# Kernel tuning notes

Hardware: AMD Instinct MI355X
Metric: run time of the kernel (lower is better)

Reference implementation:

```python
import jax, jax.numpy as jnp
import numpy as np

DIM = 768
H = 12
HD = 64  # head_dim = dim // num_heads
SCALE = HD ** (-0.5)
EPS = 1e-6


def setup_inputs() -> dict:
    key = jax.random.key(0)
    k1, k2, k3, k4, k5 = jax.random.split(key, 5)
    B, N = 8, 1024
    x = jax.random.normal(k1, (B, N, DIM), dtype=jnp.float32)
    policy = jax.random.uniform(k2, (B, N, 1), dtype=jnp.float32)
    # nn.Linear weights: [out_features, in_features]; qkv_bias=False, proj has bias
    qkv_w = jax.random.normal(k3, (3 * H * HD, DIM), dtype=jnp.float32) * (DIM ** -0.5)
    proj_w = jax.random.normal(k4, (DIM, H * HD), dtype=jnp.float32) * ((H * HD) ** -0.5)
    proj_b = jax.random.normal(k5, (DIM,), dtype=jnp.float32) * 0.01
    return {"x": x, "policy": policy, "qkv_w": qkv_w, "proj_w": proj_w, "proj_b": proj_b}


def _softmax_with_policy(attn, policy):
    # attn: [B,H,N,N], policy: [B,N,1]
    B, Hh, N, _ = attn.shape
    attn_policy = policy.reshape(B, 1, 1, N)
    eye = jnp.eye(N, dtype=attn_policy.dtype).reshape(1, 1, N, N)
    attn_policy = attn_policy + (1.0 - attn_policy) * eye
    max_att = jnp.max(attn, axis=-1, keepdims=True)
    a = jnp.exp((attn - max_att).astype(jnp.float32)) * attn_policy.astype(jnp.float32)
    a = (a + EPS / N) / (jnp.sum(a, axis=-1, keepdims=True) + EPS)
    return a.astype(max_att.dtype)


def reference(x, policy, qkv_w, proj_w, proj_b):
    B, N, C = x.shape
    qkv = (x @ qkv_w.T).reshape(B, N, 3, H, HD)
    qkv = jnp.transpose(qkv, (2, 0, 3, 1, 4))  # [3,B,H,N,HD]
    q, k, v = qkv[0], qkv[1], qkv[2]
    attn = jnp.einsum('bhnd,bhmd->bhnm', q * SCALE, k)  # [B,H,N,N]
    attn = _softmax_with_policy(attn, policy)
    out = jnp.einsum('bhnm,bhmd->bhnd', attn, v)  # [B,H,N,HD]
    out = jnp.transpose(out, (0, 2, 1, 3)).reshape(B, N, H * HD)
    return out @ proj_w.T + proj_b
```

## Files before the change

kernel.cpp:

```cpp
#include <hip/hip_runtime.h>

typedef __bf16 bf16x8 __attribute__((ext_vector_type(8)));
typedef float floatx4 __attribute__((ext_vector_type(4)));

#define EPSF 1e-6f

__device__ inline unsigned short f2bf(float f) {
  union { float f; unsigned u; } x; x.f = f;
  unsigned r = x.u + 0x7FFFu + ((x.u >> 16) & 1u);
  return (unsigned short)(r >> 16);
}
__device__ inline float bf2f(unsigned short u) {
  union { unsigned u; float f; } x; x.u = ((unsigned)u) << 16;
  return x.f;
}
__device__ inline unsigned pk2bf(float lo, float hi) {
  union { float f; unsigned u; } a, b; a.f = lo; b.f = hi;
  unsigned ua = a.u + 0x8000u, ub = b.u + 0x8000u;
  return (ub & 0xFFFF0000u) | (ua >> 16);
}
__device__ inline float fexp2(float x) { return __builtin_amdgcn_exp2f(x); }

__device__ inline floatx4 mfma16(bf16x8 a, bf16x8 b, floatx4 c) {
  return __builtin_amdgcn_mfma_f32_16x16x32_bf16(a, b, c, 0, 0, 0);
}

__device__ inline void gll16(const unsigned short* g, unsigned short* l) {
  __builtin_amdgcn_global_load_lds((__attribute__((address_space(1))) void*)g,
                                   (__attribute__((address_space(3))) void*)l, 16, 0, 0);
}

__device__ __host__ inline int sigma_inv(int p) {
  const int qq = p >> 3, jj = p & 7;
  return (jj < 4) ? (qq * 4 + jj) : (16 + qq * 4 + jj - 4);
}

__global__ __launch_bounds__(256) void prep_kernel(const float* __restrict__ x,
                                                   const float* __restrict__ qkv_w,
                                                   const float* __restrict__ proj_w,
                                                   const float* __restrict__ policy,
                                                   unsigned short* __restrict__ xb,
                                                   unsigned short* __restrict__ wqkv,
                                                   unsigned short* __restrict__ wproj,
                                                   unsigned short* __restrict__ pbf) {
  const int bid = blockIdx.x, tid = threadIdx.x;
  if (bid < 3072) {
    const int i = bid * 2048 + tid * 8;
    float4 v0 = *(const float4*)(x + i);
    float4 v1 = *(const float4*)(x + i + 4);
    __align__(16) unsigned short o[8] = {f2bf(v0.x), f2bf(v0.y), f2bf(v0.z), f2bf(v0.w),
                                         f2bf(v1.x), f2bf(v1.y), f2bf(v1.z), f2bf(v1.w)};
    *(float4*)(xb + i) = *(float4*)o;
  } else if (bid < 3936) {
    const int i = (bid - 3072) * 2048 + tid * 8;
    const float s = (i < 589824) ? 0.18033688011112042f : 1.0f;
    float4 v0 = *(const float4*)(qkv_w + i);
    float4 v1 = *(const float4*)(qkv_w + i + 4);
    __align__(16) unsigned short o[8] = {
        f2bf(v0.x * s), f2bf(v0.y * s), f2bf(v0.z * s), f2bf(v0.w * s),
        f2bf(v1.x * s), f2bf(v1.y * s), f2bf(v1.z * s), f2bf(v1.w * s)};
    *(float4*)(wqkv + i) = *(float4*)o;
  } else if (bid < 4224) {
    const int i0 = (bid - 3936) * 2048 + tid * 8;
    const int base = (i0 / 768) * 768 + ((i0 % 768) & ~63);
    __align__(16) unsigned short o[8];
#pragma unroll
    for (int t = 0; t < 8; t++) {
      const int cp = (i0 + t) & 63;
      const int c = 16 * (cp & 3) + (cp >> 2);
      o[t] = f2bf(proj_w[base + c]);
    }
    *(float4*)(wproj + i0) = *(float4*)o;
  } else {
    const int idx = (bid - 4224) * 256 + tid;
    const int b = idx >> 10, g = idx & 1023;
    const int c = ((g >> 5) << 5) + sigma_inv(g & 31);
    pbf[idx] = f2bf(policy[b * 1024 + c]);
  }
}

template <int EP, int BN>
__global__ __launch_bounds__(256, 3) void gemm_bt(const unsigned short* __restrict__ A,
                                                  const unsigned short* __restrict__ Bt,
                                                  void* __restrict__ Cout,
                                                  const float* __restrict__ bias,
                                                  int M, int N, int K) {
  constexpr int J = BN / 32;
  __shared__ __align__(16) unsigned short sA[2][128 * 32];
  __shared__ __align__(16) unsigned short sB[2][BN * 32];
  const int m0 = blockIdx.y * 128, n0 = blockIdx.x * BN;
  const int tid = threadIdx.x;
  const int lane = tid & 63, wave = tid >> 6;
  const int qd = lane >> 4, l15 = lane & 15;
  const int wr = (wave >> 1) * 64, wc = (wave & 1) * (BN / 2);
  const int srow = tid >> 2;
  const int scb = (tid & 3) ^ (srow & 3);
  const unsigned short* Ag = A + (long)(m0 + srow) * K + scb * 8;
  const unsigned short* Bg = Bt + (long)(n0 + srow) * K + scb * 8;
  const int x3 = l15 & 3;
  const int nit = K / 32;
  floatx4 acc[4][J] = {};
  gll16(Ag, &sA[0][wave * 512]);
  gll16(Ag + (long)64 * K, &sA[0][2048 + wave * 512]);
  gll16(Bg, &sB[0][wave * 512]);
  if (BN == 128) gll16(Bg + (long)64 * K, &sB[0][2048 + wave * 512]);
  __builtin_amdgcn_s_waitcnt(0);
  __syncthreads();
  for (int it = 0; it < nit; ++it) {
    const int buf = it & 1;
    if (it + 1 < nit) {
      const long k0 = 32 * (it + 1);
      gll16(Ag + k0, &sA[buf ^ 1][wave * 512]);
      gll16(Ag + (long)64 * K + k0, &sA[buf ^ 1][2048 + wave * 512]);
      gll16(Bg + k0, &sB[buf ^ 1][wave * 512]);
      if (BN == 128) gll16(Bg + (long)64 * K + k0, &sB[buf ^ 1][2048 + wave * 512]);
    }
    const int cw = (qd ^ x3) * 8;
    bf16x8 af[4], bf[J];
#pragma unroll
    for (int i = 0; i < 4; i++) af[i] = *(const bf16x8*)&sA[buf][(wr + i * 16 + l15) * 32 + cw];
#pragma unroll
    for (int j = 0; j < J; j++) bf[j] = *(const bf16x8*)&sB[buf][(wc + j * 16 + l15) * 32 + cw];
#pragma unroll
    for (int i = 0; i < 4; i++)
#pragma unroll
      for (int j = 0; j < J; j++) acc[i][j] = mfma16(af[i], bf[j], acc[i][j]);
    __builtin_amdgcn_s_waitcnt(0);
    __syncthreads();
  }
  if constexpr (EP == 0) {
#pragma unroll
    for (int i = 0; i < 4; i++)
#pragma unroll
      for (int r = 0; r < 4; r++) {
        const int row = m0 + wr + i * 16 + qd * 4 + r;
        __align__(8) unsigned short pk[4];
#pragma unroll
        for (int j = 0; j < 4; j++) pk[j] = f2bf(acc[i][j][r]);
        *(uint2*)((unsigned short*)Cout + (long)row * N + n0 + wc + 4 * l15) = *(uint2*)pk;
      }
  } else {
#pragma unroll
    for (int i = 0; i < 4; i++)
#pragma unroll
      for (int j = 0; j < J; j++) {
        const int col = n0 + wc + j * 16 + l15;
#pragma unroll
        for (int r = 0; r < 4; r++) {
          const int row = m0 + wr + i * 16 + qd * 4 + r;
          ((float*)Cout)[(long)row * N + col] = acc[i][j][r] + bias[col];
        }
      }
  }
}

__global__ __launch_bounds__(256) void transpose_v(const unsigned short* __restrict__ qkv,
                                                   const float* __restrict__ policy,
                                                   unsigned short* __restrict__ vTp) {
  __shared__ unsigned short tile[64][72];
  __shared__ float sPol[64];
  const int bh = blockIdx.y;
  const int b = bh / 12, h = bh % 12;
  const int n0 = blockIdx.x * 64;
  const int t = threadIdx.x;
  if (t < 64) sPol[t] = policy[b * 1024 + n0 + t];
  {
    const int nr = t >> 2, dc = (t & 3) * 16;
    const unsigned short* src = qkv + (long)(b * 1024 + n0 + nr) * 2304 + 2 * 768 + h * 64 + dc;
    float4 v0 = *(const float4*)src;
    float4 v1 = *(const float4*)(src + 8);
    *(float4*)&tile[nr][dc] = v0;
    *(float4*)&tile[nr][dc + 8] = v1;
  }
  __syncthreads();
  {
    const int d = t >> 2, nc = (t & 3) * 16;
    __align__(16) unsigned short o[16];
#pragma unroll
    for (int jj = 0; jj < 16; jj++) {
      const int cc = nc + jj;
      const int cl = (cc & 32) + sigma_inv(cc & 31);
      o[jj] = f2bf(bf2f(tile[cl][d]) * sPol[cl]);
    }
    unsigned short* dst = vTp + (long)(bh * 64 + d) * 1024 + n0 + nc;
    *(float4*)dst = *(float4*)&o[0];
    *(float4*)(dst + 8) = *(float4*)&o[8];
  }
}

__global__ __launch_bounds__(256, 3) void attn_kernel(const unsigned short* __restrict__ qkv,
                                                      const unsigned short* __restrict__ vTp,
                                                      const unsigned short* __restrict__ pbf,
                                                      const float* __restrict__ policy,
                                                      unsigned short* __restrict__ aout) {
  __shared__ __align__(16) unsigned short sK[2][4096];
  __shared__ __align__(16) unsigned short sV[2][4096];
  __shared__ __align__(16) unsigned short sPv[1024];
  __shared__ float sD[4][32];
  const int bid = blockIdx.x;
  const int bh = bid % 96, qt = bid / 96;
  const int b = bh / 12, h = bh % 12;
  const int tid = threadIdx.x;
  const int wave = tid >> 6, lane = tid & 63;
  const int qd = lane >> 4, l15 = lane & 15;
  const int q0 = qt * 128 + wave * 32;
  const unsigned short* qb = qkv + (long)(b * 1024 + q0 + l15) * 2304 + h * 64 + qd * 8;
  bf16x8 qf00 = *(const bf16x8*)qb;
  bf16x8 qf01 = *(const bf16x8*)(qb + 32);
  bf16x8 qf10 = *(const bf16x8*)(qb + (long)16 * 2304);
  bf16x8 qf11 = *(const bf16x8*)(qb + (long)16 * 2304 + 32);
  if (tid < 128) *(float4*)(sPv + tid * 8) = *(const float4*)(pbf + b * 1024 + tid * 8);
  const int krow = wave * 8 + (lane >> 3);
  const int kcb = (lane & 7) ^ (lane >> 3);
  const unsigned short* kgl = qkv + (long)(b * 1024 + krow) * 2304 + 768 + h * 64 + kcb * 8;
  const int vrow = tid >> 2;
  const int vcb = (tid & 3) ^ ((vrow ^ (vrow >> 2)) & 3);
  const unsigned short* vgl = vTp + (long)(bh * 64 + vrow) * 1024 + vcb * 8;
  const int x7 = l15 & 7;
  const int vsw = (qd ^ ((l15 ^ (l15 >> 2)) & 3)) * 8;
  floatx4 O0[4] = {}, O1[4] = {};
  floatx4 Dl0 = {}, Dl1 = {};
  gll16(kgl, &sK[0][wave * 512]);
  gll16(kgl + (long)32 * 2304, &sK[0][2048 + wave * 512]);
  gll16(vgl, &sV[0][wave * 512]);
  gll16(vgl + 32, &sV[0][2048 + wave * 512]);
  __builtin_amdgcn_s_waitcnt(0);
  __syncthreads();
  for (int it = 0; it < 16; ++it) {
    const int buf = it & 1;
    if (it < 15) {
      const long cn = 64 * (it + 1);
      gll16(kgl + cn * 2304, &sK[buf ^ 1][wave * 512]);
      gll16(kgl + (cn + 32) * 2304, &sK[buf ^ 1][2048 + wave * 512]);
      gll16(vgl + cn, &sV[buf ^ 1][wave * 512]);
      gll16(vgl + cn + 32, &sV[buf ^ 1][2048 + wave * 512]);
    }
    const int c0 = it * 64;
#pragma unroll
    for (int g = 0; g < 2; g++) {
      bf16x8 k00 = *(const bf16x8*)&sK[buf][((g * 2 + 0) * 16 + l15) * 64 + ((0 + qd) ^ x7) * 8];
      bf16x8 k01 = *(const bf16x8*)&sK[buf][((g * 2 + 0) * 16 + l15) * 64 + ((4 + qd) ^ x7) * 8];
      bf16x8 k10 = *(const bf16x8*)&sK[buf][((g * 2 + 1) * 16 + l15) * 64 + ((0 + qd) ^ x7) * 8];
      bf16x8 k11 = *(const bf16x8*)&sK[buf][((g * 2 + 1) * 16 + l15) * 64 + ((4 + qd) ^ x7) * 8];
      bf16x8 pv = *(const bf16x8*)&sPv[c0 + g * 32 + qd * 8];
      floatx4 z = {0.f, 0.f, 0.f, 0.f};
      floatx4 tA0 = mfma16(k01, qf01, mfma16(k00, qf00, z));
      floatx4 tB0 = mfma16(k11, qf01, mfma16(k10, qf00, z));
      floatx4 tA1 = mfma16(k01, qf11, mfma16(k00, qf10, z));
      floatx4 tB1 = mfma16(k11, qf11, mfma16(k10, qf10, z));
      uint4 pu0, pu1;
      pu0.x = pk2bf(fexp2(tA0[0]), fexp2(tA0[1]));
      pu0.y = pk2bf(fexp2(tA0[2]), fexp2(tA0[3]));
      pu0.z = pk2bf(fexp2(tB0[0]), fexp2(tB0[1]));
      pu0.w = pk2bf(fexp2(tB0[2]), fexp2(tB0[3]));
      pu1.x = pk2bf(fexp2(tA1[0]), fexp2(tA1[1]));
      pu1.y = pk2bf(fexp2(tA1[2]), fexp2(tA1[3]));
      pu1.z = pk2bf(fexp2(tB1[0]), fexp2(tB1[1]));
      pu1.w = pk2bf(fexp2(tB1[2]), fexp2(tB1[3]));
      bf16x8 pf0 = *(bf16x8*)&pu0;
      bf16x8 pf1 = *(bf16x8*)&pu1;
      bf16x8 vf0 = *(const bf16x8*)&sV[buf][g * 2048 + (0 * 16 + l15) * 32 + vsw];
      bf16x8 vf1 = *(const bf16x8*)&sV[buf][g * 2048 + (1 * 16 + l15) * 32 + vsw];
      bf16x8 vf2 = *(const bf16x8*)&sV[buf][g * 2048 + (2 * 16 + l15) * 32 + vsw];
      bf16x8 vf3 = *(const bf16x8*)&sV[buf][g * 2048 + (3 * 16 + l15) * 32 + vsw];
      Dl0 = mfma16(pf0, pv, Dl0);
      Dl1 = mfma16(pf1, pv, Dl1);
      O0[0] = mfma16(pf0, vf0, O0[0]); O1[0] = mfma16(pf1, vf0, O1[0]);
      O0[1] = mfma16(pf0, vf1, O0[1]); O1[1] = mfma16(pf1, vf1, O1[1]);
      O0[2] = mfma16(pf0, vf2, O0[2]); O1[2] = mfma16(pf1, vf2, O1[2]);
      O0[3] = mfma16(pf0, vf3, O0[3]); O1[3] = mfma16(pf1, vf3, O1[3]);
    }
    __builtin_amdgcn_s_waitcnt(0);
    __syncthreads();
  }
  {
    const unsigned short* kd = qkv + (long)(b * 1024 + q0 + l15) * 2304 + 768 + h * 64 + qd * 8;
    bf16x8 kd00 = *(const bf16x8*)kd;
    bf16x8 kd01 = *(const bf16x8*)(kd + 32);
    bf16x8 kd10 = *(const bf16x8*)(kd + (long)16 * 2304);
    bf16x8 kd11 = *(const bf16x8*)(kd + (long)16 * 2304 + 32);
    float part0 = 0.f, part1 = 0.f;
#pragma unroll
    for (int jj = 0; jj < 8; jj++) {
      part0 += (float)qf00[jj] * (float)kd00[jj] + (float)qf01[jj] * (float)kd01[jj];
      part1 += (float)qf10[jj] * (float)kd10[jj] + (float)qf11[jj] * (float)kd11[jj];
    }
    part0 += __shfl_xor(part0, 16); part0 += __shfl_xor(part0, 32);
    part1 += __shfl_xor(part1, 16); part1 += __shfl_xor(part1, 32);
    const float p0 = policy[b * 1024 + q0 + l15];
    const float p1 = policy[b * 1024 + q0 + 16 + l15];
    if (qd == 0) {
      sD[wave][l15] = fexp2(part0) * (1.0f - p0);
      sD[wave][16 + l15] = fexp2(part1) * (1.0f - p1);
    }
    __builtin_amdgcn_s_waitcnt(0);
    const unsigned short* vdiag = qkv + (long)(b * 1024 + q0) * 2304 + 1536 + h * 64 + l15;
#pragma unroll
    for (int r = 0; r < 4; r++) {
      const int row = qd * 4 + r;
      const float c0v = sD[wave][row], c1v = sD[wave][16 + row];
#pragma unroll
      for (int j = 0; j < 4; j++) {
        O0[j][r] += c0v * bf2f(vdiag[(long)row * 2304 + j * 16]);
        O1[j][r] += c1v * bf2f(vdiag[(long)(16 + row) * 2304 + j * 16]);
      }
      Dl0[r] += c0v;
      Dl1[r] += c1v;
    }
  }
  const long ob = (long)(b * 1024 + q0 + qd * 4) * 768 + h * 64 + l15;
#pragma unroll
  for (int r = 0; r < 4; r++) {
    const float li0 = 1.0f / (Dl0[r] + EPSF);
    const float li1 = 1.0f / (Dl1[r] + EPSF);
#pragma unroll
    for (int j = 0; j < 4; j++) {
      aout[ob + (long)r * 768 + j * 16] = f2bf(O0[j][r] * li0);
      aout[ob + (long)(16 * 768) + r * 768 + j * 16] = f2bf(O1[j][r] * li1);
    }
  }
}

extern "C" void kernel_launch(void* const* d_in, const int* in_sizes, int n_in,
                              void* d_out, int out_size, void* d_ws, size_t ws_size,
                              hipStream_t stream) {
  const float* x      = (const float*)d_in[0];
  const float* policy = (const float*)d_in[1];
  const float* qkv_w  = (const float*)d_in[2];
  const float* proj_w = (const float*)d_in[3];
  const float* proj_b = (const float*)d_in[4];
  float* out = (float*)d_out;

  char* ws = (char*)d_ws;
  unsigned short* xb    = (unsigned short*)(ws + 0);
  unsigned short* wqkv  = (unsigned short*)(ws + 12582912);
  unsigned short* wproj = (unsigned short*)(ws + 16121856);
  unsigned short* qkvb  = (unsigned short*)(ws + 17301504);
  unsigned short* vTp   = (unsigned short*)(ws + 55050240);
  unsigned short* aoutb = (unsigned short*)(ws + 67633152);
  unsigned short* pbf   = (unsigned short*)(ws + 80216064);

  prep_kernel<<<4256, 256, 0, stream>>>(x, qkv_w, proj_w, policy, xb, wqkv, wproj, pbf);
  gemm_bt<0, 128><<<dim3(18, 64), 256, 0, stream>>>(xb, wqkv, qkvb, nullptr, 8192, 2304, 768);
  transpose_v<<<dim3(16, 96), 256, 0, stream>>>(qkvb, policy, vTp);
  attn_kernel<<<dim3(768), 256, 0, stream>>>(qkvb, vTp, pbf, policy, aoutb);
  gemm_bt<1, 64><<<dim3(12, 64), 256, 0, stream>>>(aoutb, wproj, out, proj_b, 8192, 768, 768);
}
```

Baseline: 197.8 us.

## Replace double-buffered K=32 GEMM loop with single-buffered K=64 tiles

The bf16 GEMM main loop drops the two-stage double-buffered LDS pipeline with 32-wide K slices. It now uses a single LDS buffer holding 64-wide K slices, with a wider XOR swizzle and two MFMA sub-steps per tile. The aim is to halve the number of barrier/waitcnt rounds per K and to raise occupancy (launch bounds 4 for the QKV GEMM). In exchange, global loads no longer overlap the MFMA compute inside a block and now rely on other resident blocks to hide latency.

```diff
diff --git a/kernel.cpp b/kernel.cpp
--- a/kernel.cpp
+++ b/kernel.cpp
@@ -79,54 +79,46 @@
   }
 }
 
-template <int EP, int BN>
-__global__ __launch_bounds__(256, 3) void gemm_bt(const unsigned short* __restrict__ A,
+template <int EP, int BN, int W>
+__global__ __launch_bounds__(256, W) void gemm_bt(const unsigned short* __restrict__ A,
                                                   const unsigned short* __restrict__ Bt,
                                                   void* __restrict__ Cout,
                                                   const float* __restrict__ bias,
                                                   int M, int N, int K) {
   constexpr int J = BN / 32;
-  __shared__ __align__(16) unsigned short sA[2][128 * 32];
-  __shared__ __align__(16) unsigned short sB[2][BN * 32];
+  __shared__ __align__(16) unsigned short sA[128 * 64];
+  __shared__ __align__(16) unsigned short sB[BN * 64];
   const int m0 = blockIdx.y * 128, n0 = blockIdx.x * BN;
   const int tid = threadIdx.x;
   const int lane = tid & 63, wave = tid >> 6;
   const int qd = lane >> 4, l15 = lane & 15;
   const int wr = (wave >> 1) * 64, wc = (wave & 1) * (BN / 2);
-  const int srow = tid >> 2;
-  const int scb = (tid & 3) ^ (srow & 3);
+  const int srow = tid >> 3;
+  const int scb = (tid & 7) ^ (srow & 7);
   const unsigned short* Ag = A + (long)(m0 + srow) * K + scb * 8;
   const unsigned short* Bg = Bt + (long)(n0 + srow) * K + scb * 8;
-  const int x3 = l15 & 3;
-  const int nit = K / 32;
+  const int x7 = l15 & 7;
   floatx4 acc[4][J] = {};
-  gll16(Ag, &sA[0][wave * 512]);
-  gll16(Ag + (long)64 * K, &sA[0][2048 + wave * 512]);
-  gll16(Bg, &sB[0][wave * 512]);
-  if (BN == 128) gll16(Bg + (long)64 * K, &sB[0][2048 + wave * 512]);
-  __builtin_amdgcn_s_waitcnt(0);
-  __syncthreads();
-  for (int it = 0; it < nit; ++it) {
-    const int buf = it & 1;
-    if (it + 1 < nit) {
-      const long k0 = 32 * (it + 1);
-      gll16(Ag + k0, &sA[buf ^ 1][wave * 512]);
-      gll16(Ag + (long)64 * K + k0, &sA[buf ^ 1][2048 + wave * 512]);
-      gll16(Bg + k0, &sB[buf ^ 1][wave * 512]);
-      if (BN == 128) gll16(Bg + (long)64 * K + k0, &sB[buf ^ 1][2048 + wave * 512]);
-    }
-    const int cw = (qd ^ x3) * 8;
-    bf16x8 af[4], bf[J];
-#pragma unroll
-    for (int i = 0; i < 4; i++) af[i] = *(const bf16x8*)&sA[buf][(wr + i * 16 + l15) * 32 + cw];
-#pragma unroll
-    for (int j = 0; j < J; j++) bf[j] = *(const bf16x8*)&sB[buf][(wc + j * 16 + l15) * 32 + cw];
-#pragma unroll
-    for (int i = 0; i < 4; i++)
-#pragma unroll
-      for (int j = 0; j < J; j++) acc[i][j] = mfma16(af[i], bf[j], acc[i][j]);
-    __builtin_amdgcn_s_waitcnt(0);
+  for (int k0 = 0; k0 < K; k0 += 64) {
     __syncthreads();
+#pragma unroll
+    for (int p = 0; p < 4; p++) gll16(Ag + (long)(p * 32) * K + k0, sA + p * 2048 + wave * 512);
+#pragma unroll
+    for (int p = 0; p < J; p++) gll16(Bg + (long)(p * 32) * K + k0, sB + p * 2048 + wave * 512);
+    __syncthreads();
+#pragma unroll
+    for (int s = 0; s < 2; s++) {
+      const int cw = ((s * 4 + qd) ^ x7) * 8;
+      bf16x8 af[4], bf[J];
+#pragma unroll
+      for (int i = 0; i < 4; i++) af[i] = *(const bf16x8*)&sA[(wr + i * 16 + l15) * 64 + cw];
+#pragma unroll
+      for (int j = 0; j < J; j++) bf[j] = *(const bf16x8*)&sB[(wc + j * 16 + l15) * 64 + cw];
+#pragma unroll
+      for (int i = 0; i < 4; i++)
+#pragma unroll
+        for (int j = 0; j < J; j++) acc[i][j] = mfma16(af[i], bf[j], acc[i][j]);
+    }
   }
   if constexpr (EP == 0) {
 #pragma unroll
@@ -341,8 +333,8 @@
   unsigned short* pbf   = (unsigned short*)(ws + 80216064);
 
   prep_kernel<<<4256, 256, 0, stream>>>(x, qkv_w, proj_w, policy, xb, wqkv, wproj, pbf);
-  gemm_bt<0, 128><<<dim3(18, 64), 256, 0, stream>>>(xb, wqkv, qkvb, nullptr, 8192, 2304, 768);
+  gemm_bt<0, 128, 4><<<dim3(18, 64), 256, 0, stream>>>(xb, wqkv, qkvb, nullptr, 8192, 2304, 768);
   transpose_v<<<dim3(16, 96), 256, 0, stream>>>(qkvb, policy, vTp);
   attn_kernel<<<dim3(768), 256, 0, stream>>>(qkvb, vTp, pbf, policy, aoutb);
-  gemm_bt<1, 64><<<dim3(12, 64), 256, 0, stream>>>(aoutb, wproj, out, proj_b, 8192, 768, 768);
-}
+  gemm_bt<1, 64, 3><<<dim3(12, 64), 256, 0, stream>>>(aoutb, wproj, out, proj_b, 8192, 768, 768);
+}
```

New measurement: 190.0 us. 1.04x faster.
